# Optimization experiments

Measured on AMD Instinct MI355X. Metric: run time of the kernel, lower is better.

Reference implementation:

```python
import jax, jax.numpy as jnp
import numpy as np

N, C = 262144, 128

def setup_inputs() -> dict:
    key = jax.random.key(0)
    k1, k2 = jax.random.split(key)
    x = jax.random.normal(k1, (N, C), dtype=jnp.float32)
    # binary label matrix (0/1 floats), as implied by the _target[i][0]==0 check
    target = jax.random.randint(k2, (N, C), 0, 2).astype(jnp.float32)
    return {"x": x, "target": target}

def reference(x, target):
    # Per-row argmax over classes (torch.max(_input[i], 0) -> idx)
    idx = jnp.argmax(x, axis=1)                      # [N]
    # Rows where idx > 0 and target[i,0] == 0 get all non-idx target entries zeroed
    cond = (idx > 0) & (target[:, 0] == 0)           # [N]
    keep = jax.nn.one_hot(idx, x.shape[1], dtype=target.dtype)  # [N, C]
    t = jnp.where(cond[:, None], target * keep, target)
    return jnp.mean(jnp.abs(x * t))
```

## Files before the change

kernel.cpp:

```cpp
#include <hip/hip_runtime.h>

#define NROWS 262144
#define NCOLS 128
#define TPB 256
#define WPB (TPB / 64)
#define NBLOCKS 4096
#define NWAVES (NBLOCKS * WPB)
#define NPAIRS (NROWS / 2)
#define U 2
#define NBATCH (NPAIRS / (NWAVES * U))

typedef float floatx4 __attribute__((ext_vector_type(4)));

__device__ __forceinline__ floatx4 ntload4(const float* p)
{
    return __builtin_nontemporal_load((const floatx4*)p);
}

__global__ __launch_bounds__(TPB) void biased_loss_partial(
    const float* __restrict__ x, const float* __restrict__ t,
    float* __restrict__ partial)
{
    const int lane = threadIdx.x & 63;
    const int waveInBlock = threadIdx.x >> 6;
    const int gw = blockIdx.x * WPB + waveInBlock;
    const int half = lane >> 5;
    const int sub  = lane & 31;
    const int c    = sub * 4;

    const size_t laneoff = (size_t)half * NCOLS + (size_t)c;

    float acc = 0.0f;

    floatx4 xv[U], tv[U];
    floatx4 xn[U], tn[U];

    {
        const int pbase = gw * U;
        #pragma unroll
        for (int u = 0; u < U; ++u) {
            const size_t base = (size_t)(2 * (pbase + u)) * NCOLS + laneoff;
            xv[u] = ntload4(x + base);
            tv[u] = ntload4(t + base);
        }
    }

    #pragma unroll
    for (int b = 0; b < NBATCH; ++b) {
        if (b + 1 < NBATCH) {
            const int pbase = ((b + 1) * NWAVES + gw) * U;
            #pragma unroll
            for (int u = 0; u < U; ++u) {
                const size_t base = (size_t)(2 * (pbase + u)) * NCOLS + laneoff;
                xn[u] = ntload4(x + base);
                tn[u] = ntload4(t + base);
            }
        }

        #pragma unroll
        for (int u = 0; u < U; ++u) {
            float bv = xv[u].x; int bi = c;
            if (xv[u].y > bv) { bv = xv[u].y; bi = c + 1; }
            if (xv[u].z > bv) { bv = xv[u].z; bi = c + 2; }
            if (xv[u].w > bv) { bv = xv[u].w; bi = c + 3; }

            #pragma unroll
            for (int off = 16; off > 0; off >>= 1) {
                float ov = __shfl_xor(bv, off, 64);
                int   oi = __shfl_xor(bi, off, 64);
                if (ov > bv || (ov == bv && oi < bi)) { bv = ov; bi = oi; }
            }

            float t0 = __shfl(tv[u].x, half << 5, 64);
            const bool cond = (bi > 0) && (t0 == 0.0f);

            float c0 = fabsf(xv[u].x * tv[u].x);
            float c1 = fabsf(xv[u].y * tv[u].y);
            float c2 = fabsf(xv[u].z * tv[u].z);
            float c3 = fabsf(xv[u].w * tv[u].w);

            float s;
            if (cond) {
                s = (c     == bi ? c0 : 0.0f)
                  + (c + 1 == bi ? c1 : 0.0f)
                  + (c + 2 == bi ? c2 : 0.0f)
                  + (c + 3 == bi ? c3 : 0.0f);
            } else {
                s = (c0 + c1) + (c2 + c3);
            }
            acc += s;
        }

        if (b + 1 < NBATCH) {
            #pragma unroll
            for (int u = 0; u < U; ++u) { xv[u] = xn[u]; tv[u] = tn[u]; }
        }
    }

    #pragma unroll
    for (int off = 32; off > 0; off >>= 1)
        acc += __shfl_xor(acc, off, 64);

    __shared__ float smem[WPB];
    if (lane == 0) smem[waveInBlock] = acc;
    __syncthreads();
    if (threadIdx.x == 0) {
        float bsum = 0.0f;
        #pragma unroll
        for (int w = 0; w < WPB; ++w) bsum += smem[w];
        partial[blockIdx.x] = bsum;
    }
}

__global__ __launch_bounds__(256) void reduce_partials(
    const float* __restrict__ partial, float* __restrict__ out, int n)
{
    float acc = 0.0f;
    for (int i = threadIdx.x; i < n; i += 256) acc += partial[i];
    #pragma unroll
    for (int off = 32; off > 0; off >>= 1)
        acc += __shfl_xor(acc, off, 64);
    __shared__ float smem[4];
    const int lane = threadIdx.x & 63, w = threadIdx.x >> 6;
    if (lane == 0) smem[w] = acc;
    __syncthreads();
    if (threadIdx.x == 0) {
        float s = smem[0] + smem[1] + smem[2] + smem[3];
        out[0] = s / (float)((size_t)NROWS * (size_t)NCOLS);
    }
}

extern "C" void kernel_launch(void* const* d_in, const int* in_sizes, int n_in,
                              void* d_out, int out_size, void* d_ws, size_t ws_size,
                              hipStream_t stream) {
    const float* x = (const float*)d_in[0];
    const float* t = (const float*)d_in[1];
    float* partial = (float*)d_ws;

    biased_loss_partial<<<NBLOCKS, TPB, 0, stream>>>(x, t, partial);
    reduce_partials<<<1, 256, 0, stream>>>(partial, (float*)d_out, NBLOCKS);
}
```

Before: 253.8 us.

## Fuse final reduction via last-block atomic and simplify argmax to max+ballot

Replaces the two-kernel partial-sum plus reduce scheme with a single kernel in which the last block to finish, detected through an atomic counter, sums all partials. The counter is reset with a memset on the stream, so a kernel launch is traded for a memset plus an atomic and fences. The per-row argmax no longer shuffles value/index pairs: it reduces only the max, then uses a ballot and find-first-set to locate the first lane holding it. This roughly halves the shuffle work. The kernel is memory bound, so the arithmetic savings are likely secondary.

```diff
diff --git a/kernel.cpp b/kernel.cpp
--- a/kernel.cpp
+++ b/kernel.cpp
@@ -17,9 +17,10 @@
     return __builtin_nontemporal_load((const floatx4*)p);
 }
 
-__global__ __launch_bounds__(TPB) void biased_loss_partial(
+__global__ __launch_bounds__(TPB) void biased_loss_fused(
     const float* __restrict__ x, const float* __restrict__ t,
-    float* __restrict__ partial)
+    float* __restrict__ partial, unsigned int* __restrict__ counter,
+    float* __restrict__ out)
 {
     const int lane = threadIdx.x & 63;
     const int waveInBlock = threadIdx.x >> 6;
@@ -59,33 +60,34 @@
 
         #pragma unroll
         for (int u = 0; u < U; ++u) {
-            float bv = xv[u].x; int bi = c;
-            if (xv[u].y > bv) { bv = xv[u].y; bi = c + 1; }
-            if (xv[u].z > bv) { bv = xv[u].z; bi = c + 2; }
-            if (xv[u].w > bv) { bv = xv[u].w; bi = c + 3; }
+            const float lm = fmaxf(fmaxf(xv[u].x, xv[u].y),
+                                   fmaxf(xv[u].z, xv[u].w));
 
+            float M = lm;
             #pragma unroll
-            for (int off = 16; off > 0; off >>= 1) {
-                float ov = __shfl_xor(bv, off, 64);
-                int   oi = __shfl_xor(bi, off, 64);
-                if (ov > bv || (ov == bv && oi < bi)) { bv = ov; bi = oi; }
-            }
+            for (int off = 16; off > 0; off >>= 1)
+                M = fmaxf(M, __shfl_xor(M, off, 64));
 
-            float t0 = __shfl(tv[u].x, half << 5, 64);
-            const bool cond = (bi > 0) && (t0 == 0.0f);
+            const float tb_local = (xv[u].x == M) ? tv[u].x :
+                                   (xv[u].y == M) ? tv[u].y :
+                                   (xv[u].z == M) ? tv[u].z : tv[u].w;
 
-            float c0 = fabsf(xv[u].x * tv[u].x);
-            float c1 = fabsf(xv[u].y * tv[u].y);
-            float c2 = fabsf(xv[u].z * tv[u].z);
-            float c3 = fabsf(xv[u].w * tv[u].w);
+            const unsigned long long mask = __ballot(lm == M);
+            const unsigned int mh = (unsigned int)(mask >> (half << 5));
+            const int L = (half << 5) + (__ffs(mh) - 1);
+
+            const float x0 = __shfl(xv[u].x, half << 5, 64);
+            const float t0 = __shfl(tv[u].x, half << 5, 64);
+            const bool cond = (x0 != M) && (t0 == 0.0f);
 
             float s;
             if (cond) {
-                s = (c     == bi ? c0 : 0.0f)
-                  + (c + 1 == bi ? c1 : 0.0f)
-                  + (c + 2 == bi ? c2 : 0.0f)
-                  + (c + 3 == bi ? c3 : 0.0f);
+                s = (lane == L) ? fabsf(M) * tb_local : 0.0f;
             } else {
+                const float c0 = fabsf(xv[u].x * tv[u].x);
+                const float c1 = fabsf(xv[u].y * tv[u].y);
+                const float c2 = fabsf(xv[u].z * tv[u].z);
+                const float c3 = fabsf(xv[u].w * tv[u].w);
                 s = (c0 + c1) + (c2 + c3);
             }
             acc += s;
@@ -102,6 +104,7 @@
         acc += __shfl_xor(acc, off, 64);
 
     __shared__ float smem[WPB];
+    __shared__ int isLast;
     if (lane == 0) smem[waveInBlock] = acc;
     __syncthreads();
     if (threadIdx.x == 0) {
@@ -109,24 +112,26 @@
         #pragma unroll
         for (int w = 0; w < WPB; ++w) bsum += smem[w];
         partial[blockIdx.x] = bsum;
+        __threadfence();
+        const unsigned int prev = atomicAdd(counter, 1u);
+        isLast = (prev == NBLOCKS - 1);
     }
-}
+    __syncthreads();
 
-__global__ __launch_bounds__(256) void reduce_partials(
-    const float* __restrict__ partial, float* __restrict__ out, int n)
-{
-    float acc = 0.0f;
-    for (int i = threadIdx.x; i < n; i += 256) acc += partial[i];
-    #pragma unroll
-    for (int off = 32; off > 0; off >>= 1)
-        acc += __shfl_xor(acc, off, 64);
-    __shared__ float smem[4];
-    const int lane = threadIdx.x & 63, w = threadIdx.x >> 6;
-    if (lane == 0) smem[w] = acc;
-    __syncthreads();
-    if (threadIdx.x == 0) {
-        float s = smem[0] + smem[1] + smem[2] + smem[3];
-        out[0] = s / (float)((size_t)NROWS * (size_t)NCOLS);
+    if (isLast) {
+        __threadfence();
+        float r = 0.0f;
+        for (int i = threadIdx.x; i < NBLOCKS; i += TPB) r += partial[i];
+        #pragma unroll
+        for (int off = 32; off > 0; off >>= 1)
+            r += __shfl_xor(r, off, 64);
+        __shared__ float smem2[WPB];
+        if (lane == 0) smem2[waveInBlock] = r;
+        __syncthreads();
+        if (threadIdx.x == 0) {
+            const float s2 = smem2[0] + smem2[1] + smem2[2] + smem2[3];
+            out[0] = s2 / (float)((size_t)NROWS * (size_t)NCOLS);
+        }
     }
 }
 
@@ -136,7 +141,9 @@
     const float* x = (const float*)d_in[0];
     const float* t = (const float*)d_in[1];
     float* partial = (float*)d_ws;
+    unsigned int* counter = (unsigned int*)(partial + NBLOCKS);
 
-    biased_loss_partial<<<NBLOCKS, TPB, 0, stream>>>(x, t, partial);
-    reduce_partials<<<1, 256, 0, stream>>>(partial, (float*)d_out, NBLOCKS);
+    hipMemsetAsync((void*)counter, 0, sizeof(unsigned int), stream);
+    biased_loss_fused<<<NBLOCKS, TPB, 0, stream>>>(x, t, partial, counter,
+                                                   (float*)d_out);
 }
```

Result: slower. 457.4 us (+80.2%).
